# Optimization experiments

Measured on AMD Instinct MI355X. Metric: run time of the kernel, lower is better.

## Reference

```python
import jax, jax.numpy as jnp
import numpy as np

NEG_SLOPE = 0.2
F_OUT = 64


def setup_inputs() -> dict:
    key = jax.random.key(0)
    k1, k2, k3 = jax.random.split(key, 3)
    N, F_IN = 8192, 256
    h = jax.random.normal(k1, (N, F_IN), dtype=jnp.float32)
    adj = jnp.ones((N, N), dtype=jnp.bool_)  # unused by the original forward
    # xavier-uniform-ish init scale
    W = jax.random.uniform(k2, (F_IN, F_OUT), dtype=jnp.float32,
                           minval=-1.0, maxval=1.0) * np.sqrt(6.0 / (F_IN + F_OUT))
    a = jax.random.uniform(k3, (2 * F_OUT, 1), dtype=jnp.float32,
                           minval=-1.0, maxval=1.0) * np.sqrt(6.0 / (2 * F_OUT + 1))
    return {"h": h, "adj": adj, "W": W, "a": a}


def reference(h, adj, W, a):
    # Wh: [N, F_OUT]
    Wh = h @ W
    # The torch code materializes an [N*N, F] repeat to compute what is just
    # a broadcast add of two projected score vectors:
    # e[i, j] = leakyrelu(Wh[i] @ a1 + Wh[j] @ a2)
    s1 = Wh @ a[:F_OUT]   # [N, 1]
    s2 = Wh @ a[F_OUT:]   # [N, 1]
    e = s1 + s2.T         # [N, N]
    e = jnp.where(e >= 0, e, NEG_SLOPE * e)  # LeakyReLU(0.2)
    attention = jax.nn.softmax(e, axis=1)    # note: adj is NOT used (matches source)
    return attention @ Wh                    # [N, F_OUT]
```

## Files before the change

kernel.cpp:

```cpp
#include <hip/hip_runtime.h>
#include <math.h>

#define GN 8192
#define GF 64
#define GFIN 256
#define NEG 0.2f
#define NFINE 256
#define FCH 32

#define OFF_WH   0
#define OFF_S1   (GN*GF)
#define OFF_S2   (OFF_S1 + GN)
#define OFF_ZS   (OFF_S2 + GN)
#define OFF_IDX  (OFF_ZS + GN)
#define OFF_FA   (OFF_IDX + GN)
#define OFF_FB   (OFF_FA + NFINE*GF)
#define OFF_FSA  (OFF_FB + NFINE*GF)
#define OFF_FSB  (OFF_FSA + NFINE)
#define OFF_OFA  (OFF_FSB + NFINE)
#define OFF_OFB  (OFF_OFA + NFINE*GF)
#define OFF_OSA  (OFF_OFB + NFINE*GF)
#define OFF_OSB  (OFF_OSA + NFINE)
#define ZERO_CNT (2*NFINE*GF + 2*NFINE)

__global__ __launch_bounds__(256) void k_wh(const float* __restrict__ h,
        const float* __restrict__ W, const float* __restrict__ a,
        float* __restrict__ wsf) {
    float* Wh = wsf + OFF_WH;
    float* s1 = wsf + OFF_S1;
    float* s2 = wsf + OFF_S2;
    __shared__ float Wl[GFIN*GF];
    int t = threadIdx.x, b = blockIdx.x;
    int lane = t & 63;
    int zm = b*256 + t;
    if (zm < ZERO_CNT) wsf[OFF_FA + zm] = 0.f;
    const float4* W4 = (const float4*)W;
    float4* Wl4 = (float4*)Wl;
    #pragma unroll
    for (int m = 0; m < 16; ++m) Wl4[t + m*256] = W4[t + m*256];
    __syncthreads();
    int wid = __builtin_amdgcn_readfirstlane(t >> 6);
    int row0 = b*32 + wid*8;
    const float* hrow = h + (size_t)row0 * GFIN;
    float acc[8] = {0.f,0.f,0.f,0.f,0.f,0.f,0.f,0.f};
    #pragma unroll 8
    for (int k = 0; k < GFIN; ++k) {
        float wv = Wl[k*GF + lane];
        #pragma unroll
        for (int q = 0; q < 8; ++q) acc[q] += hrow[q*GFIN + k] * wv;
    }
    float a1 = a[lane], a2 = a[GF + lane];
    #pragma unroll
    for (int q = 0; q < 8; ++q) {
        int row = row0 + q;
        Wh[(size_t)row*GF + lane] = acc[q];
        float v1 = acc[q]*a1, v2 = acc[q]*a2;
        #pragma unroll
        for (int o = 32; o > 0; o >>= 1) { v1 += __shfl_xor(v1, o); v2 += __shfl_xor(v2, o); }
        if (lane == 0) { s1[row] = v1; s2[row] = v2; }
    }
}

__global__ __launch_bounds__(512) void k_rank(const float* __restrict__ Whg,
        float* __restrict__ wsf) {
    __shared__ float zl[GN];
    __shared__ int rl[32];
    __shared__ float redm[8];
    const float* s2 = wsf + OFF_S2;
    float* zs = wsf + OFF_ZS;
    int* idx = (int*)(wsf + OFF_IDX);
    float* fineA = wsf + OFF_FA;
    float* fineB = wsf + OFF_FB;
    float* fSA = wsf + OFF_FSA;
    float* fSB = wsf + OFF_FSB;
    int t = threadIdx.x, b = blockIdx.x;
    int lane = t & 63, wid = t >> 6;
    const float4* s4 = (const float4*)s2;
    float4* z4 = (float4*)zl;
    float mx = -1e30f;
    for (int m = t; m < GN/4; m += 512) {
        float4 v = s4[m]; z4[m] = v;
        mx = fmaxf(fmaxf(mx, v.x), fmaxf(fmaxf(v.y, v.z), v.w));
    }
    #pragma unroll
    for (int o = 32; o > 0; o >>= 1) mx = fmaxf(mx, __shfl_xor(mx, o));
    if (lane == 0) redm[wid] = mx;
    __syncthreads();
    float Z = redm[0];
    #pragma unroll
    for (int w2 = 1; w2 < 8; ++w2) Z = fmaxf(Z, redm[w2]);
    int jl = t >> 4, sl = t & 15;
    int j = b*32 + jl;
    float zj = zl[j];
    int cnt = 0;
    #pragma unroll 4
    for (int i = 0; i < GN/64; ++i) {
        int m4 = i*16 + sl;
        float4 v = z4[m4];
        int mb = m4*4;
        cnt += (v.x < zj) || (v.x == zj && mb   < j);
        cnt += (v.y < zj) || (v.y == zj && mb+1 < j);
        cnt += (v.z < zj) || (v.z == zj && mb+2 < j);
        cnt += (v.w < zj) || (v.w == zj && mb+3 < j);
    }
    cnt += __shfl_xor(cnt, 1);
    cnt += __shfl_xor(cnt, 2);
    cnt += __shfl_xor(cnt, 4);
    cnt += __shfl_xor(cnt, 8);
    if (sl == 0) { zs[cnt] = zj; idx[cnt] = j; rl[jl] = cnt; }
    __syncthreads();
    #pragma unroll
    for (int q = 0; q < 4; ++q) {
        int jj = wid*4 + q;
        int jg = b*32 + jj;
        int r = rl[jj];
        float d = zl[jg] - Z;
        float tA = __expf(d);
        float tB = __expf(NEG*d);
        float w = Whg[(size_t)jg*GF + lane];
        int fc = r >> 5;
        atomicAdd(&fineA[fc*GF + lane], tA*w);
        atomicAdd(&fineB[fc*GF + lane], tB*w);
        if (lane == 0) atomicAdd(&fSA[fc], tA);
        if (lane == 1) atomicAdd(&fSB[fc], tB);
    }
}

__global__ __launch_bounds__(256) void k_scan(float* __restrict__ wsf) {
    __shared__ float stg[NFINE];
    __shared__ float wred[4];
    const float* fineA = wsf + OFF_FA;
    const float* fineB = wsf + OFF_FB;
    const float* fSA = wsf + OFF_FSA;
    const float* fSB = wsf + OFF_FSB;
    float* ofA = wsf + OFF_OFA;
    float* ofB = wsf + OFF_OFB;
    float* osA = wsf + OFF_OSA;
    float* osB = wsf + OFF_OSB;
    int c = blockIdx.x;
    int t = threadIdx.x, lane = t & 63, wid = t >> 6;
    float fA = (c < 64) ? fineA[t*GF + c] : fSA[t];
    float fB = (c < 64) ? fineB[t*GF + c] : fSB[t];
    {
        float ws = fB;
        #pragma unroll
        for (int o = 1; o < 64; o <<= 1) { float y = __shfl_up(ws, o); if (lane >= o) ws += y; }
        if (lane == 63) wred[wid] = ws;
        __syncthreads();
        float blkoff = 0.f;
        #pragma unroll
        for (int w2 = 0; w2 < 4; ++w2) { float x = wred[w2]; if (w2 < wid) blkoff += x; }
        float exB = blkoff + ws - fB;
        if (c < 64) ofB[t*GF + c] = exB; else osB[t] = exB;
    }
    __syncthreads();
    stg[t] = fA;
    __syncthreads();
    {
        int rt = NFINE-1-t;
        float vA = stg[rt];
        float ws = vA;
        #pragma unroll
        for (int o = 1; o < 64; o <<= 1) { float y = __shfl_up(ws, o); if (lane >= o) ws += y; }
        __syncthreads();
        if (lane == 63) wred[wid] = ws;
        __syncthreads();
        float blkoff = 0.f;
        #pragma unroll
        for (int w2 = 0; w2 < 4; ++w2) { float x = wred[w2]; if (w2 < wid) blkoff += x; }
        float exA = blkoff + ws - vA;
        if (c < 64) ofA[rt*GF + c] = exA; else osA[rt] = exA;
    }
}

__global__ __launch_bounds__(256) void k_out(const float* __restrict__ wsf,
        float* __restrict__ out) {
    const float* Wh = wsf + OFF_WH;
    const float* s1 = wsf + OFF_S1;
    const float* zs = wsf + OFF_ZS;
    const int* idx = (const int*)(wsf + OFF_IDX);
    const float* ofA = wsf + OFF_OFA;
    const float* ofB = wsf + OFF_OFB;
    const float* osA = wsf + OFF_OSA;
    const float* osB = wsf + OFF_OSB;
    int t = threadIdx.x;
    int wid = t >> 6, lane = t & 63;
    int i = blockIdx.x*4 + wid;
    float s1i = s1[i];
    float Z = zs[GN-1];
    float g = s1i + Z;
    float m = (g >= 0.f) ? g : NEG*g;
    float aA = __expf(g - m);
    float aB = __expf(NEG*g - m);
    float tgt = -s1i;
    int lo = 0, hi = GN;
    #pragma unroll
    for (int it = 0; it < 13; ++it) {
        int mid = (lo + hi) >> 1;
        if (zs[mid] < tgt) lo = mid + 1; else hi = mid;
    }
    int k = lo;
    int fc = __builtin_amdgcn_readfirstlane(min(k >> 5, NFINE-1));
    float va = ofA[fc*GF + lane];
    float vb = ofB[fc*GF + lane];
    float sa = osA[fc], pb = osB[fc];
    #pragma unroll 8
    for (int q = 0; q < FCH; ++q) {
        int r = fc*FCH + q;
        float zr = zs[r];
        int ir = idx[r];
        float w = Wh[(size_t)ir*GF + lane];
        float d = zr - Z;
        if (r >= k) { float tA = __expf(d);     va += tA*w; sa += tA; }
        else        { float tB = __expf(NEG*d); vb += tB*w; pb += tB; }
    }
    out[(size_t)i*GF + lane] = (aA*va + aB*vb) / (aA*sa + aB*pb);
}

extern "C" void kernel_launch(void* const* d_in, const int* in_sizes, int n_in,
                              void* d_out, int out_size, void* d_ws, size_t ws_size,
                              hipStream_t stream) {
    const float* h = (const float*)d_in[0];
    const float* W = (const float*)d_in[2];
    const float* a = (const float*)d_in[3];
    float* wsf = (float*)d_ws;
    float* out = (float*)d_out;

    hipLaunchKernelGGL(k_wh,   dim3(GN/32), dim3(256), 0, stream, h, W, a, wsf);
    hipLaunchKernelGGL(k_rank, dim3(GN/32), dim3(512), 0, stream, wsf + OFF_WH, wsf);
    hipLaunchKernelGGL(k_scan, dim3(65),    dim3(256), 0, stream, wsf);
    hipLaunchKernelGGL(k_out,  dim3(GN/4),  dim3(256), 0, stream, wsf, out);
}
```

Before: 72.62 us.

## Replace prefix-scan kernel with two-level coarse/fine sums computed in output kernel

Removes the separate k_scan launch. k_rank now also atomically accumulates 16 coarse bucket sums, and each output row rebuilds its prefix and suffix sums from up to 15 coarse plus 15 fine bucket entries. The per-row binary search shrinks from 13 probes over all sorted keys in global memory to 8 probes over 256 chunk-max keys staged in shared memory. The cost is extra atomics in k_rank and about 30 extra loads per row in k_out, in exchange for one fewer launch and a shorter search.

```diff
diff --git a/kernel.cpp b/kernel.cpp
--- a/kernel.cpp
+++ b/kernel.cpp
@@ -7,6 +7,7 @@
 #define NEG 0.2f
 #define NFINE 256
 #define FCH 32
+#define NCO 16
 
 #define OFF_WH   0
 #define OFF_S1   (GN*GF)
@@ -17,11 +18,12 @@
 #define OFF_FB   (OFF_FA + NFINE*GF)
 #define OFF_FSA  (OFF_FB + NFINE*GF)
 #define OFF_FSB  (OFF_FSA + NFINE)
-#define OFF_OFA  (OFF_FSB + NFINE)
-#define OFF_OFB  (OFF_OFA + NFINE*GF)
-#define OFF_OSA  (OFF_OFB + NFINE*GF)
-#define OFF_OSB  (OFF_OSA + NFINE)
-#define ZERO_CNT (2*NFINE*GF + 2*NFINE)
+#define OFF_CA   (OFF_FSB + NFINE)
+#define OFF_CB   (OFF_CA + NCO*GF)
+#define OFF_CSA  (OFF_CB + NCO*GF)
+#define OFF_CSB  (OFF_CSA + NCO)
+#define OFF_CKEY (OFF_CSB + NCO)
+#define ZERO_CNT (OFF_CKEY - OFF_FA)
 
 __global__ __launch_bounds__(256) void k_wh(const float* __restrict__ h,
         const float* __restrict__ W, const float* __restrict__ a,
@@ -73,6 +75,11 @@
     float* fineB = wsf + OFF_FB;
     float* fSA = wsf + OFF_FSA;
     float* fSB = wsf + OFF_FSB;
+    float* coA = wsf + OFF_CA;
+    float* coB = wsf + OFF_CB;
+    float* cSA = wsf + OFF_CSA;
+    float* cSB = wsf + OFF_CSB;
+    float* ckey = wsf + OFF_CKEY;
     int t = threadIdx.x, b = blockIdx.x;
     int lane = t & 63, wid = t >> 6;
     const float4* s4 = (const float4*)s2;
@@ -107,7 +114,10 @@
     cnt += __shfl_xor(cnt, 2);
     cnt += __shfl_xor(cnt, 4);
     cnt += __shfl_xor(cnt, 8);
-    if (sl == 0) { zs[cnt] = zj; idx[cnt] = j; rl[jl] = cnt; }
+    if (sl == 0) {
+        zs[cnt] = zj; idx[cnt] = j; rl[jl] = cnt;
+        if ((cnt & (FCH-1)) == FCH-1) ckey[cnt >> 5] = zj;
+    }
     __syncthreads();
     #pragma unroll
     for (int q = 0; q < 4; ++q) {
@@ -119,100 +129,68 @@
         float tB = __expf(NEG*d);
         float w = Whg[(size_t)jg*GF + lane];
         int fc = r >> 5;
+        int C  = r >> 9;
         atomicAdd(&fineA[fc*GF + lane], tA*w);
         atomicAdd(&fineB[fc*GF + lane], tB*w);
+        atomicAdd(&coA[C*GF + lane], tA*w);
+        atomicAdd(&coB[C*GF + lane], tB*w);
         if (lane == 0) atomicAdd(&fSA[fc], tA);
         if (lane == 1) atomicAdd(&fSB[fc], tB);
-    }
-}
-
-__global__ __launch_bounds__(256) void k_scan(float* __restrict__ wsf) {
-    __shared__ float stg[NFINE];
-    __shared__ float wred[4];
+        if (lane == 2) atomicAdd(&cSA[C], tA);
+        if (lane == 3) atomicAdd(&cSB[C], tB);
+    }
+}
+
+__global__ __launch_bounds__(256) void k_out(const float* __restrict__ wsf,
+        float* __restrict__ out) {
+    __shared__ float ck[NFINE];
+    const float* Wh = wsf + OFF_WH;
+    const float* s1 = wsf + OFF_S1;
+    const float* zs = wsf + OFF_ZS;
+    const int* idx = (const int*)(wsf + OFF_IDX);
     const float* fineA = wsf + OFF_FA;
     const float* fineB = wsf + OFF_FB;
     const float* fSA = wsf + OFF_FSA;
     const float* fSB = wsf + OFF_FSB;
-    float* ofA = wsf + OFF_OFA;
-    float* ofB = wsf + OFF_OFB;
-    float* osA = wsf + OFF_OSA;
-    float* osB = wsf + OFF_OSB;
-    int c = blockIdx.x;
-    int t = threadIdx.x, lane = t & 63, wid = t >> 6;
-    float fA = (c < 64) ? fineA[t*GF + c] : fSA[t];
-    float fB = (c < 64) ? fineB[t*GF + c] : fSB[t];
-    {
-        float ws = fB;
-        #pragma unroll
-        for (int o = 1; o < 64; o <<= 1) { float y = __shfl_up(ws, o); if (lane >= o) ws += y; }
-        if (lane == 63) wred[wid] = ws;
-        __syncthreads();
-        float blkoff = 0.f;
-        #pragma unroll
-        for (int w2 = 0; w2 < 4; ++w2) { float x = wred[w2]; if (w2 < wid) blkoff += x; }
-        float exB = blkoff + ws - fB;
-        if (c < 64) ofB[t*GF + c] = exB; else osB[t] = exB;
-    }
-    __syncthreads();
-    stg[t] = fA;
-    __syncthreads();
-    {
-        int rt = NFINE-1-t;
-        float vA = stg[rt];
-        float ws = vA;
-        #pragma unroll
-        for (int o = 1; o < 64; o <<= 1) { float y = __shfl_up(ws, o); if (lane >= o) ws += y; }
-        __syncthreads();
-        if (lane == 63) wred[wid] = ws;
-        __syncthreads();
-        float blkoff = 0.f;
-        #pragma unroll
-        for (int w2 = 0; w2 < 4; ++w2) { float x = wred[w2]; if (w2 < wid) blkoff += x; }
-        float exA = blkoff + ws - vA;
-        if (c < 64) ofA[rt*GF + c] = exA; else osA[rt] = exA;
-    }
-}
-
-__global__ __launch_bounds__(256) void k_out(const float* __restrict__ wsf,
-        float* __restrict__ out) {
-    const float* Wh = wsf + OFF_WH;
-    const float* s1 = wsf + OFF_S1;
-    const float* zs = wsf + OFF_ZS;
-    const int* idx = (const int*)(wsf + OFF_IDX);
-    const float* ofA = wsf + OFF_OFA;
-    const float* ofB = wsf + OFF_OFB;
-    const float* osA = wsf + OFF_OSA;
-    const float* osB = wsf + OFF_OSB;
+    const float* coA = wsf + OFF_CA;
+    const float* coB = wsf + OFF_CB;
+    const float* cSA = wsf + OFF_CSA;
+    const float* cSB = wsf + OFF_CSB;
+    const float* ckey = wsf + OFF_CKEY;
     int t = threadIdx.x;
     int wid = t >> 6, lane = t & 63;
+    if (t < NFINE/4) ((float4*)ck)[t] = ((const float4*)ckey)[t];
+    __syncthreads();
     int i = blockIdx.x*4 + wid;
     float s1i = s1[i];
-    float Z = zs[GN-1];
+    float Z = ck[NFINE-1];
     float g = s1i + Z;
     float m = (g >= 0.f) ? g : NEG*g;
     float aA = __expf(g - m);
     float aB = __expf(NEG*g - m);
     float tgt = -s1i;
-    int lo = 0, hi = GN;
-    #pragma unroll
-    for (int it = 0; it < 13; ++it) {
+    int lo = 0, hi = NFINE;
+    #pragma unroll
+    for (int it = 0; it < 8; ++it) {
         int mid = (lo + hi) >> 1;
-        if (zs[mid] < tgt) lo = mid + 1; else hi = mid;
-    }
-    int k = lo;
-    int fc = __builtin_amdgcn_readfirstlane(min(k >> 5, NFINE-1));
-    float va = ofA[fc*GF + lane];
-    float vb = ofB[fc*GF + lane];
-    float sa = osA[fc], pb = osB[fc];
+        if (ck[mid] < tgt) lo = mid + 1; else hi = mid;
+    }
+    int fc = __builtin_amdgcn_readfirstlane(min(lo, NFINE-1));
+    int cc = fc >> 4;
+    float va = 0.f, vb = 0.f, sa = 0.f, pb = 0.f;
+    for (int C = 0; C < cc; ++C)        { vb += coB[C*GF + lane]; pb += cSB[C]; }
+    for (int C = cc+1; C < NCO; ++C)    { va += coA[C*GF + lane]; sa += cSA[C]; }
+    for (int f = cc*16; f < fc; ++f)    { vb += fineB[f*GF + lane]; pb += fSB[f]; }
+    for (int f = fc+1; f < cc*16+16; ++f){ va += fineA[f*GF + lane]; sa += fSA[f]; }
     #pragma unroll 8
-    for (int q = 0; q < FCH; ++q) {
-        int r = fc*FCH + q;
+    for (int e = 0; e < FCH; ++e) {
+        int r = fc*FCH + e;
         float zr = zs[r];
         int ir = idx[r];
         float w = Wh[(size_t)ir*GF + lane];
         float d = zr - Z;
-        if (r >= k) { float tA = __expf(d);     va += tA*w; sa += tA; }
-        else        { float tB = __expf(NEG*d); vb += tB*w; pb += tB; }
+        if (zr >= tgt) { float tA = __expf(d);     va += tA*w; sa += tA; }
+        else           { float tB = __expf(NEG*d); vb += tB*w; pb += tB; }
     }
     out[(size_t)i*GF + lane] = (aA*va + aB*vb) / (aA*sa + aB*pb);
 }
@@ -228,6 +206,5 @@
 
     hipLaunchKernelGGL(k_wh,   dim3(GN/32), dim3(256), 0, stream, h, W, a, wsf);
     hipLaunchKernelGGL(k_rank, dim3(GN/32), dim3(512), 0, stream, wsf + OFF_WH, wsf);
-    hipLaunchKernelGGL(k_scan, dim3(65),    dim3(256), 0, stream, wsf);
     hipLaunchKernelGGL(k_out,  dim3(GN/4),  dim3(256), 0, stream, wsf, out);
 }
```

After: 167.2 us. +130.3%, slower.
